# Optimization experiments

Measured on AMD Instinct MI355X. Metric: run time of the kernel, lower is better.

## Reference

```python
import jax, jax.numpy as jnp
import numpy as np

N = 100000       # n_nodes
E = 128          # hidden_channels
R = 9            # n_relations
L = 3            # n_layers
NE = 640000      # n_edges


def setup_inputs() -> dict:
    key = jax.random.key(0)
    k = jax.random.split(key, 5)
    edge_index = jax.random.randint(k[0], (2, NE), 0, N, dtype=jnp.int64)
    edge_type = jax.random.randint(k[1], (NE,), 0, R, dtype=jnp.int64)
    embeddings = jax.random.normal(k[2], (N, E), dtype=jnp.float32)
    # per-layer weights [L, 2R, E, E] (first R = forward direction, last R = reverse)
    weights = jax.random.normal(k[3], (L, 2 * R, E, E), dtype=jnp.float32)
    biases = jax.random.normal(k[4], (L, 2 * R, E), dtype=jnp.float32)
    return {
        "edge_index": edge_index,
        "edge_type": edge_type,
        "embeddings": embeddings,
        "weights": weights,
        "biases": biases,
    }


def reference(edge_index, edge_type, embeddings, weights, biases):
    src, dst = edge_index[0], edge_index[1]
    n_nodes = embeddings.shape[0]
    n_layers, r2 = weights.shape[0], weights.shape[1]
    n_rel = r2 // 2

    hidden = embeddings
    for l in range(n_layers):
        # NB: source code resets hidden to the embeddings at the top of each
        # layer, so each layer transforms the raw embeddings. We reproduce
        # that exactly (the relu in the source is dead code: its result is
        # immediately overwritten by `hidden = output`).
        hidden = embeddings
        # Transform node features once per relation (node-level GEMM) instead
        # of per-edge: mathematically identical to gathering then matmul.
        ht = jnp.einsum('ne,reh->rnh', hidden, weights[l])  # [2R, N, E]
        # forward direction: message = W_r @ h[src] + b_r, scattered to dst
        msg_f = ht[edge_type, src] + biases[l][edge_type]          # [NE, E]
        out = jax.ops.segment_sum(msg_f, dst, num_segments=n_nodes)
        # reverse direction: message = W_{r+R} @ h[dst] + b_{r+R}, scattered to src
        msg_b = ht[edge_type + n_rel, dst] + biases[l][edge_type + n_rel]
        out = out + jax.ops.segment_sum(msg_b, src, num_segments=n_nodes)
        hidden = out
    return hidden
```

## Files before the change

### kernel.cpp

```cpp
#include <hip/hip_runtime.h>
#include <hip/hip_bf16.h>


#define E_DIM 128
#define R_REL 9
#define TN 16
#define TCH 3
#define MT_P2 392
#define SCB 1024
#define NSLICE 96

typedef __attribute__((ext_vector_type(8))) short short8v;
typedef __attribute__((ext_vector_type(4))) float f32x4;

static __device__ __forceinline__ unsigned short f2bf(float f) {
    union { float f; unsigned u; } v; v.f = f;
    unsigned u = v.u;
    return (unsigned short)((u + 0x7FFFu + ((u >> 16) & 1u)) >> 16);
}
static __device__ __forceinline__ float bf2f(unsigned short h) {
    union { unsigned u; float f; } v; v.u = ((unsigned)h) << 16;
    return v.f;
}


__global__ __launch_bounds__(256) void prep(
    const float* __restrict__ H, const float* __restrict__ W18,
    unsigned short* __restrict__ Hbf, unsigned short* __restrict__ Wt,
    long total8)
{
    const int tid = threadIdx.x;
    if (blockIdx.x < 18) {
        const int rel = blockIdx.x;
        const float* __restrict__ Wr = W18 + (size_t)rel * E_DIM * E_DIM;
#pragma unroll
        for (int k = 0; k < 8; k++) {
            int f = tid + k * 256;
            int lane = f & 63;
            int c = (f >> 6) & 1;
            int s = (f >> 7) & 3;
            int w = (f >> 9) & 3;
            int col = w * 32 + c * 16 + (lane & 15);
            int kb = s * 32 + (lane >> 4) * 8;
            short8v v;
#pragma unroll
            for (int j = 0; j < 8; j++)
                v[j] = (short)f2bf(Wr[(size_t)(kb + j) * E_DIM + col]);
            *(short8v*)(Wt + ((size_t)((((rel * 4 + w) * 4 + s) * 2 + c) * 64 + lane)) * 8) = v;
        }
    } else {
        long i = (long)(blockIdx.x - 18) * 256 + tid;
        if (i >= total8) return;
        const float4* src = (const float4*)(H + i * 8);
        float4 a = src[0], b = src[1];
        short8v o;
        o[0] = (short)f2bf(a.x); o[1] = (short)f2bf(a.y);
        o[2] = (short)f2bf(a.z); o[3] = (short)f2bf(a.w);
        o[4] = (short)f2bf(b.x); o[5] = (short)f2bf(b.y);
        o[6] = (short)f2bf(b.z); o[7] = (short)f2bf(b.w);
        *(short8v*)(Hbf + i * 8) = o;
    }
}

__global__ __launch_bounds__(256) void k_count8(
    const int* __restrict__ esrc, const int* __restrict__ edst,
    const int* __restrict__ etype, int* __restrict__ cnt, int ne, int Nn)
{
    const int oct = blockIdx.x & 7;
    const int slice = blockIdx.x >> 3;
    const int lo = (int)(((long long)oct * Nn) >> 3);
    const int hi = (int)(((long long)(oct + 1) * Nn) >> 3);
    for (int e = slice * 256 + threadIdx.x; e < ne; e += NSLICE * 256) {
        int t = etype[e], s = esrc[e], d = edst[e];
        if (d >= lo && d < hi) atomicAdd(&cnt[d * R_REL + t], 1);
        if (s >= lo && s < hi) atomicAdd(&cnt[(Nn + s) * R_REL + t], 1);
    }
}

__global__ __launch_bounds__(256) void k_scan_part(
    const int* __restrict__ cnt, int* __restrict__ loc,
    int* __restrict__ bsum, int n2)
{
    __shared__ int sh[256];
    const int tid = threadIdx.x;
    const int i0 = blockIdx.x * SCB + tid * 4;
    int v0 = 0, v1 = 0, v2 = 0, v3 = 0;
    if (i0 + 3 < n2) {
        int4 v = *(const int4*)(cnt + i0);
        v0 = v.x; v1 = v.y; v2 = v.z; v3 = v.w;
    } else {
        if (i0 + 0 < n2) v0 = cnt[i0 + 0];
        if (i0 + 1 < n2) v1 = cnt[i0 + 1];
        if (i0 + 2 < n2) v2 = cnt[i0 + 2];
        if (i0 + 3 < n2) v3 = cnt[i0 + 3];
    }
    int t = v0 + v1 + v2 + v3;
    sh[tid] = t;
    __syncthreads();
    for (int o = 1; o < 256; o <<= 1) {
        int x = (tid >= o) ? sh[tid - o] : 0;
        __syncthreads();
        sh[tid] += x;
        __syncthreads();
    }
    int excl = sh[tid] - t;
    if (tid == 255) bsum[blockIdx.x] = sh[255];
    int p0 = excl, p1 = p0 + v0, p2 = p1 + v1, p3 = p2 + v2;
    if (i0 + 3 < n2) {
        *(int4*)(loc + i0) = make_int4(p0, p1, p2, p3);
    } else {
        if (i0 + 0 < n2) loc[i0 + 0] = p0;
        if (i0 + 1 < n2) loc[i0 + 1] = p1;
        if (i0 + 2 < n2) loc[i0 + 2] = p2;
        if (i0 + 3 < n2) loc[i0 + 3] = p3;
    }
}

__global__ __launch_bounds__(256) void k_scan_mid(int* __restrict__ bsum, int nb)
{
    __shared__ int sh[256];
    __shared__ int carry;
    const int tid = threadIdx.x;
    if (tid == 0) carry = 0;
    __syncthreads();
    for (int base = 0; base < nb; base += 256) {
        int i = base + tid;
        int v = (i < nb) ? bsum[i] : 0;
        sh[tid] = v;
        __syncthreads();
        for (int o = 1; o < 256; o <<= 1) {
            int x = (tid >= o) ? sh[tid - o] : 0;
            __syncthreads();
            sh[tid] += x;
            __syncthreads();
        }
        int excl = sh[tid] - v + carry;
        int total = sh[255];
        if (i < nb) bsum[i] = excl;
        __syncthreads();
        if (tid == 0) carry += total;
        __syncthreads();
    }
}

__global__ __launch_bounds__(256) void k_scan_apply(
    const int* __restrict__ loc, const int* __restrict__ bsum,
    int* __restrict__ off, int* __restrict__ cursor, int n2)
{
    const int add = bsum[blockIdx.x];
    const int i0 = blockIdx.x * SCB + threadIdx.x * 4;
    if (i0 + 3 < n2) {
        int4 v = *(const int4*)(loc + i0);
        v.x += add; v.y += add; v.z += add; v.w += add;
        *(int4*)(off + i0) = v;
        *(int4*)(cursor + i0) = v;
    } else {
#pragma unroll
        for (int j = 0; j < 4; j++)
            if (i0 + j < n2) {
                int v = loc[i0 + j] + add;
                off[i0 + j] = v;
                cursor[i0 + j] = v;
            }
    }
}

__global__ __launch_bounds__(256) void k_fill8(
    const int* __restrict__ esrc, const int* __restrict__ edst,
    const int* __restrict__ etype, int* __restrict__ cursor,
    unsigned* __restrict__ rec, int ne, int Nn)
{
    const int oct = blockIdx.x & 7;
    const int slice = blockIdx.x >> 3;
    const int lo = (int)(((long long)oct * Nn) >> 3);
    const int hi = (int)(((long long)(oct + 1) * Nn) >> 3);
    for (int e = slice * 256 + threadIdx.x; e < ne; e += NSLICE * 256) {
        int t = etype[e], s = esrc[e], d = edst[e];
        if (d >= lo && d < hi) {
            int p = atomicAdd(&cursor[d * R_REL + t], 1);
            rec[p] = ((unsigned)t << 20) | (unsigned)s;
        }
        if (s >= lo && s < hi) {
            int p2 = atomicAdd(&cursor[(Nn + s) * R_REL + t], 1);
            rec[p2] = ((unsigned)t << 20) | (unsigned)d;
        }
    }
}

__global__ __launch_bounds__(256, 8) void fused_rgcn(
    const unsigned short* __restrict__ Hbf, const unsigned short* __restrict__ Wt,
    const float* __restrict__ B18,
    const int* __restrict__ off3, const int* __restrict__ cur3,
    const unsigned* __restrict__ rec,
    float* __restrict__ out, int Nn)
{
    __shared__ __align__(16) unsigned short Mt[TN][MT_P2];
    __shared__ float degS[2][TN][R_REL];

    const int tid = threadIdx.x;
    const int lane = tid & 63;
    const int w = tid >> 6;
    const int lr = lane & 15;
    const int lg = lane >> 4;
    const int grp = lg;
    const int gl = lr;
    const int n0 = blockIdx.x * TN;

    const short8v* wt8 = (const short8v*)Wt;
    const short8v z8 = (short8v){0, 0, 0, 0, 0, 0, 0, 0};

    f32x4 acc[2];
    acc[0] = (f32x4){0.f, 0.f, 0.f, 0.f};
    acc[1] = (f32x4){0.f, 0.f, 0.f, 0.f};

#define RMW(rk, vk, tbase)                                                    \
    {                                                                         \
        int _tl = (int)((rk) >> 20) - (tbase);                                \
        unsigned short* _mp = &Mt[w * 4 + grp][_tl * E_DIM + gl * 8];         \
        short8v _m = *(short8v*)_mp;                                          \
        _Pragma("unroll")                                                     \
        for (int _c = 0; _c < 8; _c++) {                                      \
            float _f = bf2f((unsigned short)_m[_c]) +                         \
                       bf2f((unsigned short)(vk)[_c]);                        \
            _m[_c] = (short)f2bf(_f);                                        \
        }                                                                     \
        *(short8v*)_mp = _m;                                                  \
    }

#pragma unroll 1
    for (int dir = 0; dir < 2; dir++) {
        const int jj = lg, tt = lr;
        const int gnode_j = n0 + w * 4 + jj;
        int blo = 0x7F000000, bhi = 0x7F000000;
        if (gnode_j < Nn && tt < R_REL) {
            size_t sb = ((size_t)(dir ? (Nn + gnode_j) : gnode_j)) * R_REL + tt;
            blo = off3[sb];
            bhi = cur3[sb];
            degS[dir][w * 4 + jj][tt] = (float)(bhi - blo);
        }

#pragma unroll 1
        for (int ch = 0; ch < 3; ch++) {
            const int tbase = ch * TCH;
#pragma unroll
            for (int rr = 0; rr < 4; rr++) {
                if (lane < 48)
                    *(short8v*)(&Mt[w * 4 + rr][(size_t)lane * 8]) = z8;
            }

            const int st_g = __shfl(blo, grp * 16 + tbase);
            const int en_g = __shfl(bhi, grp * 16 + tbase + TCH - 1);

            int ii = st_g;
            while (__any(ii < en_g)) {
                bool a0 = ii + 0 < en_g;
                bool a1 = ii + 1 < en_g;
                bool a2 = ii + 2 < en_g;
                bool a3 = ii + 3 < en_g;
                unsigned r0 = 0, r1 = 0, r2 = 0, r3 = 0;
                if (a0) r0 = rec[ii + 0];
                if (a1) r1 = rec[ii + 1];
                if (a2) r2 = rec[ii + 2];
                if (a3) r3 = rec[ii + 3];
                short8v v0 = z8, v1 = z8, v2 = z8, v3 = z8;
                if (a0) v0 = *(const short8v*)(Hbf + (size_t)(r0 & 0xFFFFF) * E_DIM + gl * 8);
                if (a1) v1 = *(const short8v*)(Hbf + (size_t)(r1 & 0xFFFFF) * E_DIM + gl * 8);
                if (a2) v2 = *(const short8v*)(Hbf + (size_t)(r2 & 0xFFFFF) * E_DIM + gl * 8);
                if (a3) v3 = *(const short8v*)(Hbf + (size_t)(r3 & 0xFFFFF) * E_DIM + gl * 8);
                if (a0) RMW(r0, v0, tbase);
                if (a1) RMW(r1, v1, tbase);
                if (a2) RMW(r2, v2, tbase);
                if (a3) RMW(r3, v3, tbase);
                ii += 4;
            }
            __syncthreads();

#pragma unroll
            for (int q = 0; q < TCH; q++) {
                const int rel = dir * R_REL + tbase + q;
#pragma unroll
                for (int s = 0; s < 4; s++) {
                    short8v b0 = wt8[(size_t)((((rel * 4 + w) * 4 + s) * 2 + 0) * 64) + lane];
                    short8v b1 = wt8[(size_t)((((rel * 4 + w) * 4 + s) * 2 + 1) * 64) + lane];
                    short8v a = *(const short8v*)(&Mt[lr][q * E_DIM + s * 32 + lg * 8]);
                    acc[0] = __builtin_amdgcn_mfma_f32_16x16x32_bf16(b0, a, acc[0], 0, 0, 0);
                    acc[1] = __builtin_amdgcn_mfma_f32_16x16x32_bf16(b1, a, acc[1], 0, 0, 0);
                }
            }
            __syncthreads();
        }
    }
#undef RMW

    const int gnode = n0 + lr;
    if (gnode >= Nn) return;
#pragma unroll 1
    for (int dir = 0; dir < 2; dir++) {
#pragma unroll 1
        for (int t = 0; t < R_REL; t++) {
            float dg = degS[dir][lr][t];
            if (dg != 0.f) {
                const float* brow = B18 + (size_t)(dir * R_REL + t) * E_DIM + w * 32 + lg * 4;
                float4 b0 = *(const float4*)(brow);
                float4 b1 = *(const float4*)(brow + 16);
                acc[0][0] += dg * b0.x; acc[0][1] += dg * b0.y;
                acc[0][2] += dg * b0.z; acc[0][3] += dg * b0.w;
                acc[1][0] += dg * b1.x; acc[1][1] += dg * b1.y;
                acc[1][2] += dg * b1.z; acc[1][3] += dg * b1.w;
            }
        }
    }
    float* po = out + (size_t)gnode * E_DIM + w * 32 + lg * 4;
    *(float4*)po = make_float4(acc[0][0], acc[0][1], acc[0][2], acc[0][3]);
    *(float4*)(po + 16) = make_float4(acc[1][0], acc[1][1], acc[1][2], acc[1][3]);
}


__global__ __launch_bounds__(128) void direct_edge(
    const int* __restrict__ esrc, const int* __restrict__ edst,
    const int* __restrict__ etype,
    const float* __restrict__ H, const float* __restrict__ W2,
    const float* __restrict__ B2, float* __restrict__ out, int ne)
{
    __shared__ float hs[E_DIM];
    __shared__ float hd[E_DIM];
    int e = blockIdx.x;
    if (e >= ne) return;
    int t = etype[e], s = esrc[e], d = edst[e];
    int c = threadIdx.x;
    hs[c] = H[(size_t)s * E_DIM + c];
    hd[c] = H[(size_t)d * E_DIM + c];
    __syncthreads();
    const float* Wf = W2 + (size_t)t * E_DIM * E_DIM;
    const float* Wb = W2 + (size_t)(t + R_REL) * E_DIM * E_DIM;
    float accf = B2[(size_t)t * E_DIM + c];
    float accb = B2[(size_t)(t + R_REL) * E_DIM + c];
#pragma unroll 8
    for (int k = 0; k < E_DIM; k++) {
        accf += hs[k] * Wf[(size_t)k * E_DIM + c];
        accb += hd[k] * Wb[(size_t)k * E_DIM + c];
    }
    atomicAdd(&out[(size_t)d * E_DIM + c], accf);
    atomicAdd(&out[(size_t)s * E_DIM + c], accb);
}

extern "C" void kernel_launch(void* const* d_in, const int* in_sizes, int n_in,
                              void* d_out, int out_size, void* d_ws, size_t ws_size,
                              hipStream_t stream) {
    const int* edge_index = (const int*)d_in[0];
    const int* edge_type  = (const int*)d_in[1];
    const float* emb      = (const float*)d_in[2];
    const float* weights  = (const float*)d_in[3];
    const float* biases   = (const float*)d_in[4];
    float* out = (float*)d_out;

    const int NE = in_sizes[1];
    const int Nn = in_sizes[2] / E_DIM;
    const int L  = in_sizes[3] / (2 * R_REL * E_DIM * E_DIM);

    const float* W2 = weights + (size_t)(L - 1) * 2 * R_REL * E_DIM * E_DIM;
    const float* B2 = biases  + (size_t)(L - 1) * 2 * R_REL * E_DIM;

    const int* esrc = edge_index;
    const int* edst = edge_index + NE;

    const int n3 = 2 * Nn * R_REL;
    const int nb3 = (n3 + SCB - 1) / SCB;

    auto al = [](size_t x) { return (x + 255) & ~(size_t)255; };
    const size_t hbfBytes = al((size_t)Nn * E_DIM * 2);
    const size_t wtBytes  = al((size_t)2 * R_REL * E_DIM * E_DIM * 2);
    const size_t offBytes = al((size_t)n3 * 4);
    const size_t curBytes = al((size_t)n3 * 4);
    const size_t recBytes = al((size_t)2 * NE * 4);
    const size_t bsBytes  = al((size_t)nb3 * 4);
    const size_t need = hbfBytes + wtBytes + offBytes + curBytes + recBytes + bsBytes;

    if (ws_size >= need && Nn < (1 << 20)) {
        char* p = (char*)d_ws;
        unsigned short* Hbf = (unsigned short*)p;        p += hbfBytes;
        unsigned short* Wt  = (unsigned short*)p;        p += wtBytes;
        int* off3           = (int*)p;                   p += offBytes;
        int* cur3           = (int*)p;                   p += curBytes;
        unsigned* rec       = (unsigned*)p;              p += recBytes;
        int* bsum           = (int*)p;

        const long total8 = (long)Nn * (E_DIM / 8);
        const int hblocks = (int)((total8 + 255) / 256);

        hipMemsetAsync(off3, 0, (size_t)n3 * 4, stream);
        prep<<<18 + hblocks, 256, 0, stream>>>(emb, W2, Hbf, Wt, total8);
        k_count8<<<8 * NSLICE, 256, 0, stream>>>(esrc, edst, edge_type, off3, NE, Nn);
        k_scan_part<<<nb3, 256, 0, stream>>>(off3, cur3, bsum, n3);
        k_scan_mid<<<1, 256, 0, stream>>>(bsum, nb3);
        k_scan_apply<<<nb3, 256, 0, stream>>>(cur3, bsum, off3, cur3, n3);
        k_fill8<<<8 * NSLICE, 256, 0, stream>>>(esrc, edst, edge_type,
                                                cur3, rec, NE, Nn);

        fused_rgcn<<<(Nn + TN - 1) / TN, 256, 0, stream>>>(
            Hbf, Wt, B2, off3, cur3, rec, out, Nn);
        return;
    }

    hipMemsetAsync(d_out, 0, (size_t)Nn * E_DIM * sizeof(float), stream);
    direct_edge<<<NE, 128, 0, stream>>>(esrc, edst, edge_type, emb, W2, B2, out, NE);
}
```

Baseline: 348.5 us.

## Merge prep and count kernels; make fused RGCN kernel persistent with capped grid

```diff
diff --git a/kernel.cpp b/kernel.cpp
--- a/kernel.cpp
+++ b/kernel.cpp
@@ -24,14 +24,17 @@
 }
 
 
-__global__ __launch_bounds__(256) void prep(
+__global__ __launch_bounds__(256) void prep_count(
     const float* __restrict__ H, const float* __restrict__ W18,
+    const int* __restrict__ esrc, const int* __restrict__ edst,
+    const int* __restrict__ etype,
     unsigned short* __restrict__ Hbf, unsigned short* __restrict__ Wt,
-    long total8)
+    int* __restrict__ cnt, long total8, int hblocks, int ne, int Nn)
 {
     const int tid = threadIdx.x;
-    if (blockIdx.x < 18) {
-        const int rel = blockIdx.x;
+    const int b = blockIdx.x;
+    if (b < 18) {
+        const int rel = b;
         const float* __restrict__ Wr = W18 + (size_t)rel * E_DIM * E_DIM;
 #pragma unroll
         for (int k = 0; k < 8; k++) {
@@ -48,32 +51,28 @@
                 v[j] = (short)f2bf(Wr[(size_t)(kb + j) * E_DIM + col]);
             *(short8v*)(Wt + ((size_t)((((rel * 4 + w) * 4 + s) * 2 + c) * 64 + lane)) * 8) = v;
         }
-    } else {
-        long i = (long)(blockIdx.x - 18) * 256 + tid;
+    } else if (b < 18 + hblocks) {
+        long i = (long)(b - 18) * 256 + tid;
         if (i >= total8) return;
         const float4* src = (const float4*)(H + i * 8);
-        float4 a = src[0], b = src[1];
+        float4 a = src[0], bb = src[1];
         short8v o;
         o[0] = (short)f2bf(a.x); o[1] = (short)f2bf(a.y);
         o[2] = (short)f2bf(a.z); o[3] = (short)f2bf(a.w);
-        o[4] = (short)f2bf(b.x); o[5] = (short)f2bf(b.y);
-        o[6] = (short)f2bf(b.z); o[7] = (short)f2bf(b.w);
+        o[4] = (short)f2bf(bb.x); o[5] = (short)f2bf(bb.y);
+        o[6] = (short)f2bf(bb.z); o[7] = (short)f2bf(bb.w);
         *(short8v*)(Hbf + i * 8) = o;
-    }
-}
-
-__global__ __launch_bounds__(256) void k_count8(
-    const int* __restrict__ esrc, const int* __restrict__ edst,
-    const int* __restrict__ etype, int* __restrict__ cnt, int ne, int Nn)
-{
-    const int oct = blockIdx.x & 7;
-    const int slice = blockIdx.x >> 3;
-    const int lo = (int)(((long long)oct * Nn) >> 3);
-    const int hi = (int)(((long long)(oct + 1) * Nn) >> 3);
-    for (int e = slice * 256 + threadIdx.x; e < ne; e += NSLICE * 256) {
-        int t = etype[e], s = esrc[e], d = edst[e];
-        if (d >= lo && d < hi) atomicAdd(&cnt[d * R_REL + t], 1);
-        if (s >= lo && s < hi) atomicAdd(&cnt[(Nn + s) * R_REL + t], 1);
+    } else {
+        const int c = b - 18 - hblocks;
+        const int oct = c & 7;
+        const int slice = c >> 3;
+        const int lo = (int)(((long long)oct * Nn) >> 3);
+        const int hi = (int)(((long long)(oct + 1) * Nn) >> 3);
+        for (int e = slice * 256 + tid; e < ne; e += NSLICE * 256) {
+            int t = etype[e], s = esrc[e], d = edst[e];
+            if (d >= lo && d < hi) atomicAdd(&cnt[d * R_REL + t], 1);
+            if (s >= lo && s < hi) atomicAdd(&cnt[(Nn + s) * R_REL + t], 1);
+        }
     }
 }
 
@@ -192,7 +191,7 @@
     const float* __restrict__ B18,
     const int* __restrict__ off3, const int* __restrict__ cur3,
     const unsigned* __restrict__ rec,
-    float* __restrict__ out, int Nn)
+    float* __restrict__ out, int Nn, int ntiles)
 {
     __shared__ __align__(16) unsigned short Mt[TN][MT_P2];
     __shared__ float degS[2][TN][R_REL];
@@ -204,14 +203,8 @@
     const int lg = lane >> 4;
     const int grp = lg;
     const int gl = lr;
-    const int n0 = blockIdx.x * TN;
-
+    const short8v z8 = (short8v){0, 0, 0, 0, 0, 0, 0, 0};
     const short8v* wt8 = (const short8v*)Wt;
-    const short8v z8 = (short8v){0, 0, 0, 0, 0, 0, 0, 0};
-
-    f32x4 acc[2];
-    acc[0] = (f32x4){0.f, 0.f, 0.f, 0.f};
-    acc[1] = (f32x4){0.f, 0.f, 0.f, 0.f};
 
 #define RMW(rk, vk, tbase)                                                    \
     {                                                                         \
@@ -222,97 +215,107 @@
         for (int _c = 0; _c < 8; _c++) {                                      \
             float _f = bf2f((unsigned short)_m[_c]) +                         \
                        bf2f((unsigned short)(vk)[_c]);                        \
-            _m[_c] = (short)f2bf(_f);                                        \
+            _m[_c] = (short)f2bf(_f);                                         \
         }                                                                     \
         *(short8v*)_mp = _m;                                                  \
     }
 
+    for (int tile = blockIdx.x; tile < ntiles; tile += gridDim.x) {
+        const int n0 = tile * TN;
+
+        f32x4 acc[2];
+        acc[0] = (f32x4){0.f, 0.f, 0.f, 0.f};
+        acc[1] = (f32x4){0.f, 0.f, 0.f, 0.f};
+
 #pragma unroll 1
-    for (int dir = 0; dir < 2; dir++) {
-        const int jj = lg, tt = lr;
-        const int gnode_j = n0 + w * 4 + jj;
-        int blo = 0x7F000000, bhi = 0x7F000000;
-        if (gnode_j < Nn && tt < R_REL) {
-            size_t sb = ((size_t)(dir ? (Nn + gnode_j) : gnode_j)) * R_REL + tt;
-            blo = off3[sb];
-            bhi = cur3[sb];
-            degS[dir][w * 4 + jj][tt] = (float)(bhi - blo);
-        }
+        for (int dir = 0; dir < 2; dir++) {
+            const int jj = lg, tt = lr;
+            const int gnode_j = n0 + w * 4 + jj;
+            int blo = 0x7F000000, bhi = 0x7F000000;
+            if (gnode_j < Nn && tt < R_REL) {
+                size_t sb = ((size_t)(dir ? (Nn + gnode_j) : gnode_j)) * R_REL + tt;
+                blo = off3[sb];
+                bhi = cur3[sb];
+                degS[dir][w * 4 + jj][tt] = (float)(bhi - blo);
+            }
 
 #pragma unroll 1
-        for (int ch = 0; ch < 3; ch++) {
-            const int tbase = ch * TCH;
-#pragma unroll
-            for (int rr = 0; rr < 4; rr++) {
-                if (lane < 48)
-                    *(short8v*)(&Mt[w * 4 + rr][(size_t)lane * 8]) = z8;
+            for (int ch = 0; ch < 3; ch++) {
+                const int tbase = ch * TCH;
+#pragma unroll
+                for (int rr = 0; rr < 4; rr++) {
+                    if (lane < 48)
+                        *(short8v*)(&Mt[w * 4 + rr][(size_t)lane * 8]) = z8;
+                }
+
+                const int st_g = __shfl(blo, grp * 16 + tbase);
+                const int en_g = __shfl(bhi, grp * 16 + tbase + TCH - 1);
+
+                int ii = st_g;
+                while (__any(ii < en_g)) {
+                    bool a0 = ii + 0 < en_g;
+                    bool a1 = ii + 1 < en_g;
+                    bool a2 = ii + 2 < en_g;
+                    bool a3 = ii + 3 < en_g;
+                    unsigned r0 = 0, r1 = 0, r2 = 0, r3 = 0;
+                    if (a0) r0 = rec[ii + 0];
+                    if (a1) r1 = rec[ii + 1];
+                    if (a2) r2 = rec[ii + 2];
+                    if (a3) r3 = rec[ii + 3];
+                    short8v v0 = z8, v1 = z8, v2 = z8, v3 = z8;
+                    if (a0) v0 = *(const short8v*)(Hbf + (size_t)(r0 & 0xFFFFF) * E_DIM + gl * 8);
+                    if (a1) v1 = *(const short8v*)(Hbf + (size_t)(r1 & 0xFFFFF) * E_DIM + gl * 8);
+                    if (a2) v2 = *(const short8v*)(Hbf + (size_t)(r2 & 0xFFFFF) * E_DIM + gl * 8);
+                    if (a3) v3 = *(const short8v*)(Hbf + (size_t)(r3 & 0xFFFFF) * E_DIM + gl * 8);
+                    if (a0) RMW(r0, v0, tbase);
+                    if (a1) RMW(r1, v1, tbase);
+                    if (a2) RMW(r2, v2, tbase);
+                    if (a3) RMW(r3, v3, tbase);
+                    ii += 4;
+                }
+                __syncthreads();
+
+#pragma unroll
+                for (int q = 0; q < TCH; q++) {
+                    const int rel = dir * R_REL + tbase + q;
+#pragma unroll
+                    for (int s = 0; s < 4; s++) {
+                        short8v b0 = wt8[(size_t)((((rel * 4 + w) * 4 + s) * 2 + 0) * 64) + lane];
+                        short8v b1 = wt8[(size_t)((((rel * 4 + w) * 4 + s) * 2 + 1) * 64) + lane];
+                        short8v a = *(const short8v*)(&Mt[lr][q * E_DIM + s * 32 + lg * 8]);
+                        acc[0] = __builtin_amdgcn_mfma_f32_16x16x32_bf16(b0, a, acc[0], 0, 0, 0);
+                        acc[1] = __builtin_amdgcn_mfma_f32_16x16x32_bf16(b1, a, acc[1], 0, 0, 0);
+                    }
+                }
+                __syncthreads();
             }
-
-            const int st_g = __shfl(blo, grp * 16 + tbase);
-            const int en_g = __shfl(bhi, grp * 16 + tbase + TCH - 1);
-
-            int ii = st_g;
-            while (__any(ii < en_g)) {
-                bool a0 = ii + 0 < en_g;
-                bool a1 = ii + 1 < en_g;
-                bool a2 = ii + 2 < en_g;
-                bool a3 = ii + 3 < en_g;
-                unsigned r0 = 0, r1 = 0, r2 = 0, r3 = 0;
-                if (a0) r0 = rec[ii + 0];
-                if (a1) r1 = rec[ii + 1];
-                if (a2) r2 = rec[ii + 2];
-                if (a3) r3 = rec[ii + 3];
-                short8v v0 = z8, v1 = z8, v2 = z8, v3 = z8;
-                if (a0) v0 = *(const short8v*)(Hbf + (size_t)(r0 & 0xFFFFF) * E_DIM + gl * 8);
-                if (a1) v1 = *(const short8v*)(Hbf + (size_t)(r1 & 0xFFFFF) * E_DIM + gl * 8);
-                if (a2) v2 = *(const short8v*)(Hbf + (size_t)(r2 & 0xFFFFF) * E_DIM + gl * 8);
-                if (a3) v3 = *(const short8v*)(Hbf + (size_t)(r3 & 0xFFFFF) * E_DIM + gl * 8);
-                if (a0) RMW(r0, v0, tbase);
-                if (a1) RMW(r1, v1, tbase);
-                if (a2) RMW(r2, v2, tbase);
-                if (a3) RMW(r3, v3, tbase);
-                ii += 4;
-            }
-            __syncthreads();
-
-#pragma unroll
-            for (int q = 0; q < TCH; q++) {
-                const int rel = dir * R_REL + tbase + q;
-#pragma unroll
-                for (int s = 0; s < 4; s++) {
-                    short8v b0 = wt8[(size_t)((((rel * 4 + w) * 4 + s) * 2 + 0) * 64) + lane];
-                    short8v b1 = wt8[(size_t)((((rel * 4 + w) * 4 + s) * 2 + 1) * 64) + lane];
-                    short8v a = *(const short8v*)(&Mt[lr][q * E_DIM + s * 32 + lg * 8]);
-                    acc[0] = __builtin_amdgcn_mfma_f32_16x16x32_bf16(b0, a, acc[0], 0, 0, 0);
-                    acc[1] = __builtin_amdgcn_mfma_f32_16x16x32_bf16(b1, a, acc[1], 0, 0, 0);
+        }
+
+        const int gnode = n0 + lr;
+        if (gnode < Nn) {
+#pragma unroll 1
+            for (int dir = 0; dir < 2; dir++) {
+#pragma unroll 1
+                for (int t = 0; t < R_REL; t++) {
+                    float dg = degS[dir][lr][t];
+                    if (dg != 0.f) {
+                        const float* brow = B18 + (size_t)(dir * R_REL + t) * E_DIM + w * 32 + lg * 4;
+                        float4 b0 = *(const float4*)(brow);
+                        float4 b1 = *(const float4*)(brow + 16);
+                        acc[0][0] += dg * b0.x; acc[0][1] += dg * b0.y;
+                        acc[0][2] += dg * b0.z; acc[0][3] += dg * b0.w;
+                        acc[1][0] += dg * b1.x; acc[1][1] += dg * b1.y;
+                        acc[1][2] += dg * b1.z; acc[1][3] += dg * b1.w;
+                    }
                 }
             }
-            __syncthreads();
-        }
+            float* po = out + (size_t)gnode * E_DIM + w * 32 + lg * 4;
+            *(float4*)po = make_float4(acc[0][0], acc[0][1], acc[0][2], acc[0][3]);
+            *(float4*)(po + 16) = make_float4(acc[1][0], acc[1][1], acc[1][2], acc[1][3]);
+        }
+        __syncthreads();
     }
 #undef RMW
-
-    const int gnode = n0 + lr;
-    if (gnode >= Nn) return;
-#pragma unroll 1
-    for (int dir = 0; dir < 2; dir++) {
-#pragma unroll 1
-        for (int t = 0; t < R_REL; t++) {
-            float dg = degS[dir][lr][t];
-            if (dg != 0.f) {
-                const float* brow = B18 + (size_t)(dir * R_REL + t) * E_DIM + w * 32 + lg * 4;
-                float4 b0 = *(const float4*)(brow);
-                float4 b1 = *(const float4*)(brow + 16);
-                acc[0][0] += dg * b0.x; acc[0][1] += dg * b0.y;
-                acc[0][2] += dg * b0.z; acc[0][3] += dg * b0.w;
-                acc[1][0] += dg * b1.x; acc[1][1] += dg * b1.y;
-                acc[1][2] += dg * b1.z; acc[1][3] += dg * b1.w;
-            }
-        }
-    }
-    float* po = out + (size_t)gnode * E_DIM + w * 32 + lg * 4;
-    *(float4*)po = make_float4(acc[0][0], acc[0][1], acc[0][2], acc[0][3]);
-    *(float4*)(po + 16) = make_float4(acc[1][0], acc[1][1], acc[1][2], acc[1][3]);
 }
 
 
@@ -389,16 +392,19 @@
         const int hblocks = (int)((total8 + 255) / 256);
 
         hipMemsetAsync(off3, 0, (size_t)n3 * 4, stream);
-        prep<<<18 + hblocks, 256, 0, stream>>>(emb, W2, Hbf, Wt, total8);
-        k_count8<<<8 * NSLICE, 256, 0, stream>>>(esrc, edst, edge_type, off3, NE, Nn);
+        prep_count<<<18 + hblocks + 8 * NSLICE, 256, 0, stream>>>(
+            emb, W2, esrc, edst, edge_type, Hbf, Wt, off3,
+            total8, hblocks, NE, Nn);
         k_scan_part<<<nb3, 256, 0, stream>>>(off3, cur3, bsum, n3);
         k_scan_mid<<<1, 256, 0, stream>>>(bsum, nb3);
         k_scan_apply<<<nb3, 256, 0, stream>>>(cur3, bsum, off3, cur3, n3);
         k_fill8<<<8 * NSLICE, 256, 0, stream>>>(esrc, edst, edge_type,
                                                 cur3, rec, NE, Nn);
 
-        fused_rgcn<<<(Nn + TN - 1) / TN, 256, 0, stream>>>(
-            Hbf, Wt, B2, off3, cur3, rec, out, Nn);
+        const int ntiles = (Nn + TN - 1) / TN;
+        const int pgrid = (ntiles < 2048) ? ntiles : 2048;
+        fused_rgcn<<<pgrid, 256, 0, stream>>>(
+            Hbf, Wt, B2, off3, cur3, rec, out, Nn, ntiles);
         return;
     }
 
```

After: 348.1 us. About the same (-0.1%).
